# Kernel tuning notes

Measured on AMD Instinct MI355X. Metric: run time of the kernel, lower is better.

Reference implementation:

```python
import jax, jax.numpy as jnp
import numpy as np

N_NODES = 100000
N_EDGES = 3200000
NFEAT = 256
NHID = 256


def setup_inputs() -> dict:
    key = jax.random.key(0)
    ks = jax.random.split(key, 8)
    x = jax.random.normal(ks[0], (N_NODES, NFEAT), dtype=jnp.float32)
    # Glorot-ish scaled weights
    W1 = jax.random.normal(ks[1], (NFEAT, NHID), dtype=jnp.float32) / np.sqrt(NFEAT)
    b1 = jax.random.normal(ks[2], (NHID,), dtype=jnp.float32) * 0.01
    W2 = jax.random.normal(ks[3], (NHID, NHID), dtype=jnp.float32) / np.sqrt(NHID)
    b2 = jax.random.normal(ks[4], (NHID,), dtype=jnp.float32) * 0.01
    edge_weight = jax.random.uniform(ks[5], (N_EDGES,), dtype=jnp.float32)
    edge_src = jax.random.randint(ks[6], (N_EDGES,), 0, N_NODES, dtype=jnp.int32)
    edge_dst = jax.random.randint(ks[7], (N_EDGES,), 0, N_NODES, dtype=jnp.int32)
    return {
        "x": x, "W1": W1, "b1": b1, "W2": W2, "b2": b2,
        "edge_weight": edge_weight, "edge_src": edge_src, "edge_dst": edge_dst,
    }


def _gcn_layer(x, W, b, edge_weight, edge_src, edge_dst):
    # support = x @ W  (dense GEMM, [N, d_out])
    support = x @ W
    # spmm(adj, support): gather source rows, scale by edge weight, scatter-add to dst
    msgs = support[edge_src] * edge_weight[:, None]          # [E, d_out]
    agg = jax.ops.segment_sum(msgs, edge_dst, num_segments=N_NODES)
    return agg + b


def reference(x, W1, b1, W2, b2, edge_weight, edge_src, edge_dst):
    # Eval mode: F.dropout is identity (training=False).
    h = jax.nn.elu(_gcn_layer(x, W1, b1, edge_weight, edge_src, edge_dst))
    h = jax.nn.elu(_gcn_layer(h, W2, b2, edge_weight, edge_src, edge_dst))
    return h
```

## Files before the change

kernel.cpp:

```cpp
#include <hip/hip_runtime.h>
#include <math.h>

#define N_NODES 100000
#define N_EDGES 3200000
#define NF 256

typedef unsigned short u16;
typedef unsigned int u32;

typedef __bf16 bf16x8_t __attribute__((ext_vector_type(8)));
typedef float f32x4_t __attribute__((ext_vector_type(4)));

union U8 { uint4 q; u16 s[8]; };

typedef __attribute__((address_space(1))) const void* as1_cvp;
typedef __attribute__((address_space(3))) void* as3_vp;

__device__ __forceinline__ float bf2f(u16 u) {
  union { u32 i; float f; } v; v.i = ((u32)u) << 16; return v.f;
}
__device__ __forceinline__ u16 f2bf(float f) {
  union { float f; u32 i; } v; v.f = f;
  u32 x = v.i;
  u32 r = (x + 0x7FFFu + ((x >> 16) & 1u)) >> 16;
  return (u16)r;
}
__device__ __forceinline__ float u2f(u32 u) {
  union { u32 i; float f; } v; v.i = u; return v.f;
}

__device__ __forceinline__ void gload_lds16(const u16* g, u16* l) {
  __builtin_amdgcn_global_load_lds((as1_cvp)g, (as3_vp)l, 16, 0, 0);
}

__global__ void sniff_kernel(const u16* __restrict__ xr, int* __restrict__ flag) {
  __shared__ int cnt;
  if (threadIdx.x == 0) cnt = 0;
  __syncthreads();
  int c = 0;
  for (int i = threadIdx.x; i < 65536; i += 256) {
    u16 u = xr[i];
    if ((u & 0x7F80u) == 0x7F80u) c++;
  }
  atomicAdd(&cnt, c);
  __syncthreads();
  if (threadIdx.x == 0) flag[0] = (cnt >= 4) ? 1 : 0;
}

__global__ void transpose_w(const u16* __restrict__ Wu, const float* __restrict__ Wf,
                            const int* __restrict__ flagp, u16* __restrict__ Wt) {
  int k = blockIdx.x;
  int n = threadIdx.x;
  if (flagp[0]) Wt[n * NF + k] = f2bf(Wf[k * NF + n]);
  else          Wt[n * NF + k] = Wu[k * NF + n];
}

__global__ void conv_bias(const u16* __restrict__ bu, const float* __restrict__ bf_,
                          const int* __restrict__ flagp, u16* __restrict__ o) {
  int i = threadIdx.x;
  if (flagp[0]) o[i] = f2bf(bf_[i]);
  else          o[i] = bu[i];
}

__global__ void conv_x(const float* __restrict__ xf, const int* __restrict__ flagp,
                       u16* __restrict__ xbf) {
  if (!flagp[0]) return;
  size_t i = ((size_t)blockIdx.x * 256 + threadIdx.x) * 8;
  float4 a = *(const float4*)(xf + i);
  float4 b = *(const float4*)(xf + i + 4);
  U8 t;
  t.s[0] = f2bf(a.x); t.s[1] = f2bf(a.y); t.s[2] = f2bf(a.z); t.s[3] = f2bf(a.w);
  t.s[4] = f2bf(b.x); t.s[5] = f2bf(b.y); t.s[6] = f2bf(b.z); t.s[7] = f2bf(b.w);
  *(uint4*)(xbf + i) = t.q;
}

__global__ void hist_rank(const int* __restrict__ dst, int* __restrict__ counts,
                          int* __restrict__ rank) {
  int e = blockIdx.x * 256 + threadIdx.x;
  rank[e] = atomicAdd(&counts[dst[e]], 1);
}

__global__ void scanA(const int* __restrict__ counts, int* __restrict__ partial) {
  __shared__ int s[256];
  int t = threadIdx.x;
  int gid = blockIdx.x * 256 + t;
  int v = (gid < N_NODES) ? counts[gid] : 0;
  s[t] = v;
  __syncthreads();
  for (int offd = 128; offd > 0; offd >>= 1) {
    if (t < offd) s[t] += s[t + offd];
    __syncthreads();
  }
  if (t == 0) partial[blockIdx.x] = s[0];
}

__global__ void scanB(int* __restrict__ partial) {
  const int NPART = 391;
  __shared__ int s[512];
  int t = threadIdx.x;
  int v = (t < NPART) ? partial[t] : 0;
  s[t] = v;
  __syncthreads();
  for (int offd = 1; offd < 512; offd <<= 1) {
    int x = 0;
    if (t >= offd) x = s[t - offd];
    __syncthreads();
    s[t] += x;
    __syncthreads();
  }
  if (t < NPART) partial[t] = (t == 0) ? 0 : s[t - 1];
}

__global__ void scanC(const int* __restrict__ counts, const int* __restrict__ partial,
                      int* __restrict__ offs) {
  __shared__ int s[256];
  int t = threadIdx.x;
  int b = blockIdx.x;
  int gid = b * 256 + t;
  int v = (gid < N_NODES) ? counts[gid] : 0;
  s[t] = v;
  __syncthreads();
  for (int offd = 1; offd < 256; offd <<= 1) {
    int x = 0;
    if (t >= offd) x = s[t - offd];
    __syncthreads();
    s[t] += x;
    __syncthreads();
  }
  int incl = s[t];
  if (gid < N_NODES) offs[gid] = partial[b] + (incl - v);
  if (gid == N_NODES - 1) offs[N_NODES] = partial[b] + incl;
}

__global__ void place_pack(const int* __restrict__ src, const int* __restrict__ dst,
                           const u16* __restrict__ wu, const float* __restrict__ wf,
                           const int* __restrict__ flagp, const int* __restrict__ offs,
                           const int* __restrict__ rank, uint2* __restrict__ rec) {
  int e = blockIdx.x * 256 + threadIdx.x;
  int pos = offs[dst[e]] + rank[e];
  float w = flagp[0] ? wf[e] : bf2f(wu[e]);
  uint2 r;
  r.x = (u32)src[e];
  r.y = __float_as_uint(w);
  rec[pos] = r;
}

__global__ void place_full(const int* __restrict__ src, const int* __restrict__ dst,
                           const u16* __restrict__ wu, const float* __restrict__ wf,
                           const int* __restrict__ flagp, const int* __restrict__ offs,
                           const int* __restrict__ rank,
                           int* __restrict__ ssrc, u16* __restrict__ sw) {
  int e = blockIdx.x * 256 + threadIdx.x;
  int pos = offs[dst[e]] + rank[e];
  ssrc[pos] = src[e];
  if (flagp[0]) sw[pos] = f2bf(wf[e]);
  else          sw[pos] = wu[e];
}

__global__ void place_eid(const int* __restrict__ dst, const int* __restrict__ offs,
                          const int* __restrict__ rank, int* __restrict__ seid) {
  int e = blockIdx.x * 256 + threadIdx.x;
  seid[offs[dst[e]] + rank[e]] = e;
}

__global__ __launch_bounds__(256) void gemm_gll(
    const u16* __restrict__ A0, const u16* __restrict__ A1,
    const u16* __restrict__ Bt, u16* __restrict__ C, int M,
    const int* __restrict__ flagp) {
  __shared__ __align__(16) u16 Al[128 * 32];
  __shared__ __align__(16) u16 Bl[128 * 32];
  const u16* A = flagp[0] ? A1 : A0;
  const int tid = threadIdx.x;
  const int m0 = blockIdx.x * 128;
  const int n0 = blockIdx.y * 128;
  const int lane = tid & 63;
  const int wave = tid >> 6;
  const int wm = (wave & 1) * 64;
  const int wn = (wave >> 1) * 64;
  const int mrow = lane & 15;
  const int grp = lane >> 4;

  f32x4_t acc[4][4];
  const f32x4_t zero = {0.f, 0.f, 0.f, 0.f};
#pragma unroll
  for (int i = 0; i < 4; ++i)
#pragma unroll
    for (int j = 0; j < 4; ++j) acc[i][j] = zero;

  const int rA = lane >> 2;
  const int cA = (lane & 3) * 8;

  for (int k0 = 0; k0 < NF; k0 += 32) {
#pragma unroll
    for (int c = 0; c < 2; ++c) {
      int r0 = wave * 32 + c * 16;
      int ar = r0 + rA;
      int gm = m0 + ar;
      if (gm >= M) gm = 0;
      gload_lds16(A + (size_t)gm * NF + k0 + cA, &Al[r0 * 32]);
      gload_lds16(Bt + (size_t)(n0 + ar) * NF + k0 + cA, &Bl[r0 * 32]);
    }
    __syncthreads();
    bf16x8_t af[4], bfr[4];
#pragma unroll
    for (int i = 0; i < 4; ++i)
      af[i] = *(const bf16x8_t*)(&Al[(wm + i * 16 + mrow) * 32 + grp * 8]);
#pragma unroll
    for (int j = 0; j < 4; ++j)
      bfr[j] = *(const bf16x8_t*)(&Bl[(wn + j * 16 + mrow) * 32 + grp * 8]);
#pragma unroll
    for (int i = 0; i < 4; ++i)
#pragma unroll
      for (int j = 0; j < 4; ++j)
        acc[i][j] = __builtin_amdgcn_mfma_f32_16x16x32_bf16(bfr[j], af[i], acc[i][j], 0, 0, 0);
    __syncthreads();
  }

#pragma unroll
  for (int i = 0; i < 4; ++i) {
    int row = m0 + wm + i * 16 + mrow;
    if (row >= M) continue;
#pragma unroll
    for (int j = 0; j < 4; ++j) {
      u16 pk[4];
      pk[0] = f2bf(acc[i][j][0]);
      pk[1] = f2bf(acc[i][j][1]);
      pk[2] = f2bf(acc[i][j][2]);
      pk[3] = f2bf(acc[i][j][3]);
      *(uint2*)(C + (size_t)row * NF + n0 + wn + j * 16 + grp * 4) = *(const uint2*)pk;
    }
  }
}

__global__ __launch_bounds__(256) void agg_pack(
    const u16* __restrict__ sup, const int* __restrict__ offs,
    const uint2* __restrict__ rec,
    const u16* __restrict__ bbf, u16* __restrict__ out2, float* __restrict__ out4,
    const int* __restrict__ flagp, int outmask) {
  int node = blockIdx.x * 4 + (threadIdx.x >> 6);
  int lane = threadIdx.x & 63;
  int half = lane >> 5;
  int c0 = (lane & 31) * 8;
  float a0 = 0.f, a1 = 0.f, a2 = 0.f, a3 = 0.f, a4 = 0.f, a5 = 0.f, a6 = 0.f, a7 = 0.f;
  int eend = offs[node + 1];
  int e = offs[node] + half;

  for (; e + 6 < eend; e += 8) {
    uint2 r0 = rec[e], r1 = rec[e + 2], r2 = rec[e + 4], r3 = rec[e + 6];
    float w0 = u2f(r0.y), w1 = u2f(r1.y), w2 = u2f(r2.y), w3 = u2f(r3.y);
    U8 v0, v1, v2, v3;
    v0.q = *(const uint4*)(sup + (((u32)r0.x) << 8) + c0);
    v1.q = *(const uint4*)(sup + (((u32)r1.x) << 8) + c0);
    v2.q = *(const uint4*)(sup + (((u32)r2.x) << 8) + c0);
    v3.q = *(const uint4*)(sup + (((u32)r3.x) << 8) + c0);
    a0 += bf2f(v0.s[0]) * w0; a1 += bf2f(v0.s[1]) * w0; a2 += bf2f(v0.s[2]) * w0; a3 += bf2f(v0.s[3]) * w0;
    a4 += bf2f(v0.s[4]) * w0; a5 += bf2f(v0.s[5]) * w0; a6 += bf2f(v0.s[6]) * w0; a7 += bf2f(v0.s[7]) * w0;
    a0 += bf2f(v1.s[0]) * w1; a1 += bf2f(v1.s[1]) * w1; a2 += bf2f(v1.s[2]) * w1; a3 += bf2f(v1.s[3]) * w1;
    a4 += bf2f(v1.s[4]) * w1; a5 += bf2f(v1.s[5]) * w1; a6 += bf2f(v1.s[6]) * w1; a7 += bf2f(v1.s[7]) * w1;
    a0 += bf2f(v2.s[0]) * w2; a1 += bf2f(v2.s[1]) * w2; a2 += bf2f(v2.s[2]) * w2; a3 += bf2f(v2.s[3]) * w2;
    a4 += bf2f(v2.s[4]) * w2; a5 += bf2f(v2.s[5]) * w2; a6 += bf2f(v2.s[6]) * w2; a7 += bf2f(v2.s[7]) * w2;
    a0 += bf2f(v3.s[0]) * w3; a1 += bf2f(v3.s[1]) * w3; a2 += bf2f(v3.s[2]) * w3; a3 += bf2f(v3.s[3]) * w3;
    a4 += bf2f(v3.s[4]) * w3; a5 += bf2f(v3.s[5]) * w3; a6 += bf2f(v3.s[6]) * w3; a7 += bf2f(v3.s[7]) * w3;
  }
  for (; e < eend; e += 2) {
    uint2 r0 = rec[e];
    float w0 = u2f(r0.y);
    U8 v0;
    v0.q = *(const uint4*)(sup + (((u32)r0.x) << 8) + c0);
    a0 += bf2f(v0.s[0]) * w0; a1 += bf2f(v0.s[1]) * w0; a2 += bf2f(v0.s[2]) * w0; a3 += bf2f(v0.s[3]) * w0;
    a4 += bf2f(v0.s[4]) * w0; a5 += bf2f(v0.s[5]) * w0; a6 += bf2f(v0.s[6]) * w0; a7 += bf2f(v0.s[7]) * w0;
  }

  a0 += __shfl_xor(a0, 32); a1 += __shfl_xor(a1, 32);
  a2 += __shfl_xor(a2, 32); a3 += __shfl_xor(a3, 32);
  a4 += __shfl_xor(a4, 32); a5 += __shfl_xor(a5, 32);
  a6 += __shfl_xor(a6, 32); a7 += __shfl_xor(a7, 32);

  if (half == 0) {
    U8 bv; bv.q = *(const uint4*)(bbf + c0);
    float r0 = a0 + bf2f(bv.s[0]);
    float r1 = a1 + bf2f(bv.s[1]);
    float r2 = a2 + bf2f(bv.s[2]);
    float r3 = a3 + bf2f(bv.s[3]);
    float r4 = a4 + bf2f(bv.s[4]);
    float r5 = a5 + bf2f(bv.s[5]);
    float r6 = a6 + bf2f(bv.s[6]);
    float r7 = a7 + bf2f(bv.s[7]);
    r0 = r0 > 0.f ? r0 : expm1f(r0);
    r1 = r1 > 0.f ? r1 : expm1f(r1);
    r2 = r2 > 0.f ? r2 : expm1f(r2);
    r3 = r3 > 0.f ? r3 : expm1f(r3);
    r4 = r4 > 0.f ? r4 : expm1f(r4);
    r5 = r5 > 0.f ? r5 : expm1f(r5);
    r6 = r6 > 0.f ? r6 : expm1f(r6);
    r7 = r7 > 0.f ? r7 : expm1f(r7);
    if (outmask && flagp[0]) {
      float4 o4a, o4b;
      o4a.x = r0; o4a.y = r1; o4a.z = r2; o4a.w = r3;
      o4b.x = r4; o4b.y = r5; o4b.z = r6; o4b.w = r7;
      *(float4*)(out4 + (size_t)node * NF + c0) = o4a;
      *(float4*)(out4 + (size_t)node * NF + c0 + 4) = o4b;
    } else {
      U8 o;
      o.s[0] = f2bf(r0); o.s[1] = f2bf(r1); o.s[2] = f2bf(r2); o.s[3] = f2bf(r3);
      o.s[4] = f2bf(r4); o.s[5] = f2bf(r5); o.s[6] = f2bf(r6); o.s[7] = f2bf(r7);
      *(uint4*)(out2 + (size_t)node * NF + c0) = o.q;
    }
  }
}

__global__ __launch_bounds__(256) void agg_full(
    const u16* __restrict__ sup, const int* __restrict__ offs,
    const int* __restrict__ ssrc, const u16* __restrict__ sw,
    const u16* __restrict__ bbf, u16* __restrict__ out2, float* __restrict__ out4,
    const int* __restrict__ flagp, int outmask) {
  int node = blockIdx.x * 4 + (threadIdx.x >> 6);
  int lane = threadIdx.x & 63;
  int half = lane >> 5;
  int c0 = (lane & 31) * 8;
  float a0 = 0.f, a1 = 0.f, a2 = 0.f, a3 = 0.f, a4 = 0.f, a5 = 0.f, a6 = 0.f, a7 = 0.f;
  int eend = offs[node + 1];
  int e = offs[node] + half;

  for (; e + 6 < eend; e += 8) {
    int s0 = ssrc[e], s1 = ssrc[e + 2], s2 = ssrc[e + 4], s3 = ssrc[e + 6];
    float w0 = bf2f(sw[e]), w1 = bf2f(sw[e + 2]), w2 = bf2f(sw[e + 4]), w3 = bf2f(sw[e + 6]);
    U8 v0, v1, v2, v3;
    v0.q = *(const uint4*)(sup + (((u32)s0) << 8) + c0);
    v1.q = *(const uint4*)(sup + (((u32)s1) << 8) + c0);
    v2.q = *(const uint4*)(sup + (((u32)s2) << 8) + c0);
    v3.q = *(const uint4*)(sup + (((u32)s3) << 8) + c0);
    a0 += bf2f(v0.s[0]) * w0; a1 += bf2f(v0.s[1]) * w0; a2 += bf2f(v0.s[2]) * w0; a3 += bf2f(v0.s[3]) * w0;
    a4 += bf2f(v0.s[4]) * w0; a5 += bf2f(v0.s[5]) * w0; a6 += bf2f(v0.s[6]) * w0; a7 += bf2f(v0.s[7]) * w0;
    a0 += bf2f(v1.s[0]) * w1; a1 += bf2f(v1.s[1]) * w1; a2 += bf2f(v1.s[2]) * w1; a3 += bf2f(v1.s[3]) * w1;
    a4 += bf2f(v1.s[4]) * w1; a5 += bf2f(v1.s[5]) * w1; a6 += bf2f(v1.s[6]) * w1; a7 += bf2f(v1.s[7]) * w1;
    a0 += bf2f(v2.s[0]) * w2; a1 += bf2f(v2.s[1]) * w2; a2 += bf2f(v2.s[2]) * w2; a3 += bf2f(v2.s[3]) * w2;
    a4 += bf2f(v2.s[4]) * w2; a5 += bf2f(v2.s[5]) * w2; a6 += bf2f(v2.s[6]) * w2; a7 += bf2f(v2.s[7]) * w2;
    a0 += bf2f(v3.s[0]) * w3; a1 += bf2f(v3.s[1]) * w3; a2 += bf2f(v3.s[2]) * w3; a3 += bf2f(v3.s[3]) * w3;
    a4 += bf2f(v3.s[4]) * w3; a5 += bf2f(v3.s[5]) * w3; a6 += bf2f(v3.s[6]) * w3; a7 += bf2f(v3.s[7]) * w3;
  }
  for (; e < eend; e += 2) {
    int s0 = ssrc[e];
    float w0 = bf2f(sw[e]);
    U8 v0;
    v0.q = *(const uint4*)(sup + (((u32)s0) << 8) + c0);
    a0 += bf2f(v0.s[0]) * w0; a1 += bf2f(v0.s[1]) * w0; a2 += bf2f(v0.s[2]) * w0; a3 += bf2f(v0.s[3]) * w0;
    a4 += bf2f(v0.s[4]) * w0; a5 += bf2f(v0.s[5]) * w0; a6 += bf2f(v0.s[6]) * w0; a7 += bf2f(v0.s[7]) * w0;
  }

  a0 += __shfl_xor(a0, 32); a1 += __shfl_xor(a1, 32);
  a2 += __shfl_xor(a2, 32); a3 += __shfl_xor(a3, 32);
  a4 += __shfl_xor(a4, 32); a5 += __shfl_xor(a5, 32);
  a6 += __shfl_xor(a6, 32); a7 += __shfl_xor(a7, 32);

  if (half == 0) {
    U8 bv; bv.q = *(const uint4*)(bbf + c0);
    float r0 = a0 + bf2f(bv.s[0]);
    float r1 = a1 + bf2f(bv.s[1]);
    float r2 = a2 + bf2f(bv.s[2]);
    float r3 = a3 + bf2f(bv.s[3]);
    float r4 = a4 + bf2f(bv.s[4]);
    float r5 = a5 + bf2f(bv.s[5]);
    float r6 = a6 + bf2f(bv.s[6]);
    float r7 = a7 + bf2f(bv.s[7]);
    r0 = r0 > 0.f ? r0 : expm1f(r0);
    r1 = r1 > 0.f ? r1 : expm1f(r1);
    r2 = r2 > 0.f ? r2 : expm1f(r2);
    r3 = r3 > 0.f ? r3 : expm1f(r3);
    r4 = r4 > 0.f ? r4 : expm1f(r4);
    r5 = r5 > 0.f ? r5 : expm1f(r5);
    r6 = r6 > 0.f ? r6 : expm1f(r6);
    r7 = r7 > 0.f ? r7 : expm1f(r7);
    if (outmask && flagp[0]) {
      float4 o4a, o4b;
      o4a.x = r0; o4a.y = r1; o4a.z = r2; o4a.w = r3;
      o4b.x = r4; o4b.y = r5; o4b.z = r6; o4b.w = r7;
      *(float4*)(out4 + (size_t)node * NF + c0) = o4a;
      *(float4*)(out4 + (size_t)node * NF + c0 + 4) = o4b;
    } else {
      U8 o;
      o.s[0] = f2bf(r0); o.s[1] = f2bf(r1); o.s[2] = f2bf(r2); o.s[3] = f2bf(r3);
      o.s[4] = f2bf(r4); o.s[5] = f2bf(r5); o.s[6] = f2bf(r6); o.s[7] = f2bf(r7);
      *(uint4*)(out2 + (size_t)node * NF + c0) = o.q;
    }
  }
}

__global__ __launch_bounds__(256) void agg_eid(
    const u16* __restrict__ sup, const int* __restrict__ offs,
    const int* __restrict__ seid, const int* __restrict__ esrc,
    const u16* __restrict__ ewu, const float* __restrict__ ewf,
    const u16* __restrict__ bbf, u16* __restrict__ out2, float* __restrict__ out4,
    const int* __restrict__ flagp, int outmask) {
  int node = blockIdx.x * 4 + (threadIdx.x >> 6);
  int lane = threadIdx.x & 63;
  int c0 = lane * 4;
  int isf = flagp[0];
  float a0 = 0.f, a1 = 0.f, a2 = 0.f, a3 = 0.f;
  int e = offs[node];
  int eend = offs[node + 1];
  for (; e < eend; ++e) {
    int eid = seid[e];
    int src = esrc[eid];
    float w = isf ? ewf[eid] : bf2f(ewu[eid]);
    ushort4 v = *(const ushort4*)(sup + (size_t)src * NF + c0);
    a0 += bf2f(v.x) * w;
    a1 += bf2f(v.y) * w;
    a2 += bf2f(v.z) * w;
    a3 += bf2f(v.w) * w;
  }
  ushort4 bv = *(const ushort4*)(bbf + c0);
  float r0 = a0 + bf2f(bv.x);
  float r1 = a1 + bf2f(bv.y);
  float r2 = a2 + bf2f(bv.z);
  float r3 = a3 + bf2f(bv.w);
  r0 = r0 > 0.f ? r0 : expm1f(r0);
  r1 = r1 > 0.f ? r1 : expm1f(r1);
  r2 = r2 > 0.f ? r2 : expm1f(r2);
  r3 = r3 > 0.f ? r3 : expm1f(r3);
  if (outmask && isf) {
    float4 o4;
    o4.x = r0; o4.y = r1; o4.z = r2; o4.w = r3;
    *(float4*)(out4 + (size_t)node * NF + c0) = o4;
  } else {
    ushort4 o;
    o.x = f2bf(r0); o.y = f2bf(r1); o.z = f2bf(r2); o.w = f2bf(r3);
    *(ushort4*)(out2 + (size_t)node * NF + c0) = o;
  }
}

extern "C" void kernel_launch(void* const* d_in, const int* in_sizes, int n_in,
                              void* d_out, int out_size, void* d_ws, size_t ws_size,
                              hipStream_t stream) {
  const u16* x2    = (const u16*)d_in[0];
  const float* x4  = (const float*)d_in[0];
  const u16* W1u   = (const u16*)d_in[1];
  const float* W1f = (const float*)d_in[1];
  const u16* b1u   = (const u16*)d_in[2];
  const float* b1f = (const float*)d_in[2];
  const u16* W2u   = (const u16*)d_in[3];
  const float* W2f = (const float*)d_in[3];
  const u16* b2u   = (const u16*)d_in[4];
  const float* b2f = (const float*)d_in[4];
  const u16* ewu   = (const u16*)d_in[5];
  const float* ewf = (const float*)d_in[5];
  const int* esrc  = (const int*)d_in[6];
  const int* edst  = (const int*)d_in[7];
  u16* out2  = (u16*)d_out;
  float* out4 = (float*)d_out;

  char* ws = (char*)d_ws;
  size_t oWt1     = 0;
  size_t oWt2     = 131072;
  size_t oSup     = 262144;
  size_t oCounts  = 51462144;
  size_t oOffs    = 51862528;
  size_t oPartial = 52663296;
  size_t oFlag    = 52665344;
  size_t oBb1     = 52665600;
  size_t oBb2     = 52666624;
  size_t oTail    = 52667648;
  size_t need_pack  = oTail + (size_t)N_EDGES * 8;
  size_t need_split = oTail + 12800000 + 6400000;

  u16* Wt1     = (u16*)(ws + oWt1);
  u16* Wt2     = (u16*)(ws + oWt2);
  u16* sup     = (u16*)(ws + oSup);
  int* rank    = (int*)(ws + oSup);
  int* counts  = (int*)(ws + oCounts);
  int* offs    = (int*)(ws + oOffs);
  int* partial = (int*)(ws + oPartial);
  int* flag    = (int*)(ws + oFlag);
  u16* bb1     = (u16*)(ws + oBb1);
  u16* bb2     = (u16*)(ws + oBb2);

  u16* h1  = out2;
  u16* xbf = (u16*)((char*)d_out + (size_t)N_NODES * NF * 2);

  sniff_kernel<<<1, 256, 0, stream>>>(x2, flag);
  hipMemsetAsync(counts, 0, (size_t)N_NODES * 4, stream);
  transpose_w<<<256, 256, 0, stream>>>(W1u, W1f, flag, Wt1);
  transpose_w<<<256, 256, 0, stream>>>(W2u, W2f, flag, Wt2);
  conv_bias<<<1, 256, 0, stream>>>(b1u, b1f, flag, bb1);
  conv_bias<<<1, 256, 0, stream>>>(b2u, b2f, flag, bb2);
  conv_x<<<N_NODES * NF / (256 * 8), 256, 0, stream>>>(x4, flag, xbf);
  hist_rank<<<N_EDGES / 256, 256, 0, stream>>>(edst, counts, rank);
  scanA<<<391, 256, 0, stream>>>(counts, partial);
  scanB<<<1, 512, 0, stream>>>(partial);
  scanC<<<391, 256, 0, stream>>>(counts, partial, offs);

  dim3 ggrid((N_NODES + 127) / 128, 2);

  if (ws_size >= need_pack) {
    uint2* rec = (uint2*)(ws + oTail);
    place_pack<<<N_EDGES / 256, 256, 0, stream>>>(esrc, edst, ewu, ewf, flag, offs, rank, rec);
    gemm_gll<<<ggrid, 256, 0, stream>>>(x2, xbf, Wt1, sup, N_NODES, flag);
    agg_pack<<<N_NODES / 4, 256, 0, stream>>>(sup, offs, rec, bb1, h1, out4, flag, 0);
    gemm_gll<<<ggrid, 256, 0, stream>>>(h1, h1, Wt2, sup, N_NODES, flag);
    agg_pack<<<N_NODES / 4, 256, 0, stream>>>(sup, offs, rec, bb2, out2, out4, flag, 1);
  } else if (ws_size >= need_split) {
    int* ssrc = (int*)(ws + oTail);
    u16* sw   = (u16*)(ws + oTail + 12800000);
    place_full<<<N_EDGES / 256, 256, 0, stream>>>(esrc, edst, ewu, ewf, flag, offs, rank, ssrc, sw);
    gemm_gll<<<ggrid, 256, 0, stream>>>(x2, xbf, Wt1, sup, N_NODES, flag);
    agg_full<<<N_NODES / 4, 256, 0, stream>>>(sup, offs, ssrc, sw, bb1, h1, out4, flag, 0);
    gemm_gll<<<ggrid, 256, 0, stream>>>(h1, h1, Wt2, sup, N_NODES, flag);
    agg_full<<<N_NODES / 4, 256, 0, stream>>>(sup, offs, ssrc, sw, bb2, out2, out4, flag, 1);
  } else {
    int* seid = (int*)(ws + oTail);
    place_eid<<<N_EDGES / 256, 256, 0, stream>>>(edst, offs, rank, seid);
    gemm_gll<<<ggrid, 256, 0, stream>>>(x2, xbf, Wt1, sup, N_NODES, flag);
    agg_eid<<<N_NODES / 4, 256, 0, stream>>>(sup, offs, seid, esrc, ewu, ewf, bb1, h1, out4, flag, 0);
    gemm_gll<<<ggrid, 256, 0, stream>>>(h1, h1, Wt2, sup, N_NODES, flag);
    agg_eid<<<N_NODES / 4, 256, 0, stream>>>(sup, offs, seid, esrc, ewu, ewf, bb2, out2, out4, flag, 1);
  }
}
```

Before: 989.3 us.

## Double-buffer GEMM LDS tiles and fuse weight/bias prep kernels

Merges the two weight-transpose launches and two bias-conversion launches into a single prep kernel, cutting three launches. Double-buffers the A/B LDS tiles in the GEMM so the global-to-LDS load for the next K step is issued while the current step's MFMAs run. This aims to hide load latency at the cost of twice the LDS per block, which may reduce occupancy. The GEMM is a small part of a pipeline dominated by aggregation.

After: 990.1 us. Within noise of the previous version (+0.1%).

```diff
diff --git a/kernel.cpp b/kernel.cpp
--- a/kernel.cpp
+++ b/kernel.cpp
@@ -47,19 +47,26 @@
   if (threadIdx.x == 0) flag[0] = (cnt >= 4) ? 1 : 0;
 }
 
-__global__ void transpose_w(const u16* __restrict__ Wu, const float* __restrict__ Wf,
-                            const int* __restrict__ flagp, u16* __restrict__ Wt) {
-  int k = blockIdx.x;
-  int n = threadIdx.x;
-  if (flagp[0]) Wt[n * NF + k] = f2bf(Wf[k * NF + n]);
-  else          Wt[n * NF + k] = Wu[k * NF + n];
-}
-
-__global__ void conv_bias(const u16* __restrict__ bu, const float* __restrict__ bf_,
-                          const int* __restrict__ flagp, u16* __restrict__ o) {
-  int i = threadIdx.x;
-  if (flagp[0]) o[i] = f2bf(bf_[i]);
-  else          o[i] = bu[i];
+__global__ void prep_wb(const u16* __restrict__ W1u, const float* __restrict__ W1f,
+                        const u16* __restrict__ W2u, const float* __restrict__ W2f,
+                        const u16* __restrict__ b1u, const float* __restrict__ b1f,
+                        const u16* __restrict__ b2u, const float* __restrict__ b2f,
+                        const int* __restrict__ flagp,
+                        u16* __restrict__ Wt1, u16* __restrict__ Wt2,
+                        u16* __restrict__ bb1, u16* __restrict__ bb2) {
+  int b = blockIdx.x;
+  int t = threadIdx.x;
+  int isf = flagp[0];
+  if (b < 256) {
+    Wt1[t * NF + b] = isf ? f2bf(W1f[b * NF + t]) : W1u[b * NF + t];
+  } else if (b < 512) {
+    int k = b - 256;
+    Wt2[t * NF + k] = isf ? f2bf(W2f[k * NF + t]) : W2u[k * NF + t];
+  } else if (b == 512) {
+    bb1[t] = isf ? f2bf(b1f[t]) : b1u[t];
+  } else {
+    bb2[t] = isf ? f2bf(b2f[t]) : b2u[t];
+  }
 }
 
 __global__ void conv_x(const float* __restrict__ xf, const int* __restrict__ flagp,
@@ -167,8 +174,8 @@
     const u16* __restrict__ A0, const u16* __restrict__ A1,
     const u16* __restrict__ Bt, u16* __restrict__ C, int M,
     const int* __restrict__ flagp) {
-  __shared__ __align__(16) u16 Al[128 * 32];
-  __shared__ __align__(16) u16 Bl[128 * 32];
+  __shared__ __align__(16) u16 Al[2][128 * 32];
+  __shared__ __align__(16) u16 Bl[2][128 * 32];
   const u16* A = flagp[0] ? A1 : A0;
   const int tid = threadIdx.x;
   const int m0 = blockIdx.x * 128;
@@ -189,25 +196,33 @@
 
   const int rA = lane >> 2;
   const int cA = (lane & 3) * 8;
-
-  for (int k0 = 0; k0 < NF; k0 += 32) {
+  const int r0 = wave * 32;
+
+  auto stage = [&](int buf, int k0) {
 #pragma unroll
     for (int c = 0; c < 2; ++c) {
-      int r0 = wave * 32 + c * 16;
-      int ar = r0 + rA;
+      int rr = r0 + c * 16;
+      int ar = rr + rA;
       int gm = m0 + ar;
       if (gm >= M) gm = 0;
-      gload_lds16(A + (size_t)gm * NF + k0 + cA, &Al[r0 * 32]);
-      gload_lds16(Bt + (size_t)(n0 + ar) * NF + k0 + cA, &Bl[r0 * 32]);
+      gload_lds16(A + (size_t)gm * NF + k0 + cA, &Al[buf][rr * 32]);
+      gload_lds16(Bt + (size_t)(n0 + ar) * NF + k0 + cA, &Bl[buf][rr * 32]);
     }
-    __syncthreads();
+  };
+
+  stage(0, 0);
+  __syncthreads();
+
+  for (int t = 0; t < 8; ++t) {
+    int cur = t & 1;
+    if (t < 7) stage(cur ^ 1, (t + 1) * 32);
     bf16x8_t af[4], bfr[4];
 #pragma unroll
     for (int i = 0; i < 4; ++i)
-      af[i] = *(const bf16x8_t*)(&Al[(wm + i * 16 + mrow) * 32 + grp * 8]);
+      af[i] = *(const bf16x8_t*)(&Al[cur][(wm + i * 16 + mrow) * 32 + grp * 8]);
 #pragma unroll
     for (int j = 0; j < 4; ++j)
-      bfr[j] = *(const bf16x8_t*)(&Bl[(wn + j * 16 + mrow) * 32 + grp * 8]);
+      bfr[j] = *(const bf16x8_t*)(&Bl[cur][(wn + j * 16 + mrow) * 32 + grp * 8]);
 #pragma unroll
     for (int i = 0; i < 4; ++i)
 #pragma unroll
@@ -479,10 +494,8 @@
 
   sniff_kernel<<<1, 256, 0, stream>>>(x2, flag);
   hipMemsetAsync(counts, 0, (size_t)N_NODES * 4, stream);
-  transpose_w<<<256, 256, 0, stream>>>(W1u, W1f, flag, Wt1);
-  transpose_w<<<256, 256, 0, stream>>>(W2u, W2f, flag, Wt2);
-  conv_bias<<<1, 256, 0, stream>>>(b1u, b1f, flag, bb1);
-  conv_bias<<<1, 256, 0, stream>>>(b2u, b2f, flag, bb2);
+  prep_wb<<<514, 256, 0, stream>>>(W1u, W1f, W2u, W2f, b1u, b1f, b2u, b2f,
+                                   flag, Wt1, Wt2, bb1, bb2);
   conv_x<<<N_NODES * NF / (256 * 8), 256, 0, stream>>>(x4, flag, xbf);
   hist_rank<<<N_EDGES / 256, 256, 0, stream>>>(edst, counts, rank);
   scanA<<<391, 256, 0, stream>>>(counts, partial);
```
